# Kernel tuning notes

Hardware: AMD Instinct MI355X
Metric: run time of the kernel (lower is better)

## Reference

```python
import jax, jax.numpy as jnp
import numpy as np

S = 7
M = 8        # ensemble size (num_models)
D = 1008     # AEV feature dim
N = 50400    # total atoms (single conformer), divisible by S
LAYER_DIMS = (1008, 256, 192, 160, 1)
CELU_ALPHA = 0.1


def setup_inputs() -> dict:
    key = jax.random.key(0)
    ks = jax.random.split(key, 2 + 2 * (len(LAYER_DIMS) - 1))
    # Equal-size species groups (7200 atoms per species), randomly permuted.
    sp = jnp.tile(jnp.arange(S, dtype=jnp.int32), N // S)
    sp = jax.random.permutation(ks[0], sp)[None, :]                 # [1, N]
    aev = jax.random.normal(ks[1], (1, N, D), dtype=jnp.float32)    # [1, N, D]
    inp = {"species": sp, "aev": aev}
    for i in range(len(LAYER_DIMS) - 1):
        fan_in, fan_out = LAYER_DIMS[i], LAYER_DIMS[i + 1]
        w = jax.random.normal(ks[2 + 2 * i], (S, M, fan_in, fan_out), jnp.float32) / np.float32(np.sqrt(fan_in))
        b = jax.random.normal(ks[3 + 2 * i], (S, M, 1, fan_out), jnp.float32) * 0.01
        inp[f"W{i}"] = w
        inp[f"b{i}"] = b
    return inp


def _celu(x, alpha=CELU_ALPHA):
    return jnp.where(x > 0, x, alpha * jnp.expm1(x / alpha))


def _forward(species, aev, Ws, bs):
    sp = species.reshape(-1)                         # [N]
    x = aev.reshape(-1, aev.shape[-1])               # [N, D]
    s = Ws[0].shape[0]
    n = sp.shape[0]
    g = n // s                                       # atoms per species (equal groups)
    # MoE dispatch: stable sort by species -> contiguous equal-size blocks.
    order = jnp.argsort(sp)                          # [N]
    h = x[order].reshape(s, g, -1)                   # [S, G, D]
    # Fused per-species ensemble MLP (grouped batched GEMM = baddbmm per species).
    h = jnp.einsum('sgd,smdh->smgh', h, Ws[0]) + bs[0]   # [S, M, G, H0]
    for w, b in zip(Ws[1:], bs[1:]):
        h = _celu(h)
        h = jnp.einsum('smgh,smhp->smgp', h, w) + b
    atom_e = jnp.mean(h, axis=1)                     # mean over ensemble -> [S, G, 1]
    # Combine: scatter-sum of per-atom energies -> single molecular energy.
    return jnp.sum(atom_e).reshape(1)


def reference(species, aev, W0, b0, W1, b1, W2, b2, W3, b3):
    return _forward(species, aev, (W0, W1, W2, W3), (b0, b1, b2, b3))
```

## Files before the change

### kernel.cpp

```cpp
#include <hip/hip_runtime.h>
#include <cstdint>
#include <cstddef>

typedef unsigned short u16t;
typedef __attribute__((ext_vector_type(8))) short short8;
typedef __attribute__((ext_vector_type(4))) float float4v;

#define NATOMS 50400
#define SSP    7
#define DIN    1008
#define KP     1024
#define GRP    7200
#define GPAD   7296
#define H0D    256
#define H1D    192
#define H2D    160

#define OFF_CNT   0ull
#define OFF_SRC   256ull
#define OFF_X     204544ull
#define OFF_W0T   104800000ull
#define OFF_W1T   134160128ull
#define OFF_W2T   139665152ull

__device__ __forceinline__ u16t f2bf(float f) {
    union { float f; unsigned u; } x; x.f = f;
    unsigned r = x.u + 0x7fffu + ((x.u >> 16) & 1u);
    return (u16t)(r >> 16);
}
__device__ __forceinline__ float bf2f(u16t h) {
    return __uint_as_float(((unsigned)h) << 16);
}
__device__ __forceinline__ float celu_f(float x) {
    return x > 0.f ? x : 0.1f * (__expf(x * 10.f) - 1.f);
}
__device__ __forceinline__ void gll16(const void* g, void* l) {
    __builtin_amdgcn_global_load_lds(
        (const __attribute__((address_space(1))) void*)g,
        (__attribute__((address_space(3))) void*)l, 16, 0, 0);
}


__global__ void assign_k(const int* __restrict__ sp, int* __restrict__ cnt,
                         int* __restrict__ src_of) {
    int i = blockIdx.x * 256 + threadIdx.x;
    int lane = threadIdx.x & 63;
    int s = (i < NATOMS) ? sp[i] : -1;
#pragma unroll
    for (int t = 0; t < SSP; ++t) {
        unsigned long long m = __ballot(s == t);
        if (s == t) {
            int leader = __ffsll((unsigned long long)m) - 1;
            int rank = __popcll(m & ((1ull << lane) - 1ull));
            int base = 0;
            if (lane == leader) base = atomicAdd(&cnt[t], __popcll(m));
            base = __shfl(base, leader);
            src_of[t * GPAD + base + rank] = i;
        }
    }
}

__global__ void gather_k(const float* __restrict__ aev, const int* __restrict__ src_of,
                         u16t* __restrict__ X) {
    int wv = threadIdx.x >> 6, lane = threadIdx.x & 63;
    int s = blockIdx.y;
    int r = blockIdx.x * 4 + wv;
    int b = s * GPAD + r;
    bool valid = (r < GRP);
    int src = valid ? src_of[b] : 0;
    const float* ap = aev + (size_t)src * DIN;
    u16t* xp = X + (size_t)b * KP;
#pragma unroll
    for (int j = 0; j < 2; ++j) {
        int c = (j * 64 + lane) * 8;
        short8 o = (short8){0, 0, 0, 0, 0, 0, 0, 0};
        if (valid && c < DIN) {
            float4 v0 = *(const float4*)(ap + c);
            float4 v1 = *(const float4*)(ap + c + 4);
            o[0] = (short)f2bf(v0.x); o[1] = (short)f2bf(v0.y);
            o[2] = (short)f2bf(v0.z); o[3] = (short)f2bf(v0.w);
            o[4] = (short)f2bf(v1.x); o[5] = (short)f2bf(v1.y);
            o[6] = (short)f2bf(v1.z); o[7] = (short)f2bf(v1.w);
        }
        *(short8*)(xp + c) = o;
    }
}

__global__ void transpose_convert_k(const float* __restrict__ src, u16t* __restrict__ dst,
                                    int K_in, int C, int K_out) {
    __shared__ float tile[64][65];
    int b = blockIdx.z;
    int k0 = blockIdx.x * 64, c0 = blockIdx.y * 64;
    int tx = threadIdx.x & 63, ty = threadIdx.x >> 6;
    const float* sp = src + (size_t)b * K_in * C;
#pragma unroll
    for (int i = 0; i < 16; ++i) {
        int kl = i * 4 + ty;
        int k = k0 + kl, c = c0 + tx;
        float v = (k < K_in && c < C) ? sp[(size_t)k * C + c] : 0.f;
        tile[kl][tx] = v;
    }
    __syncthreads();
    u16t* dp = dst + (size_t)b * C * K_out;
    int kq = (threadIdx.x & 15) * 4;
    int cb = threadIdx.x >> 4;
#pragma unroll
    for (int p = 0; p < 4; ++p) {
        int cl = p * 16 + cb;
        int c = c0 + cl;
        if (c < C) {
            ushort4 o;
            o.x = f2bf(tile[kq + 0][cl]); o.y = f2bf(tile[kq + 1][cl]);
            o.z = f2bf(tile[kq + 2][cl]); o.w = f2bf(tile[kq + 3][cl]);
            *(ushort4*)(dp + (size_t)c * K_out + k0 + kq) = o;
        }
    }
}

__launch_bounds__(256, 2)
__global__ void fused(const u16t* __restrict__ X, const u16t* __restrict__ W0T,
                      const u16t* __restrict__ W1T, const u16t* __restrict__ W2T,
                      const float* __restrict__ b0, const float* __restrict__ b1,
                      const float* __restrict__ b2, const float* __restrict__ b3,
                      const float* __restrict__ W3, float* __restrict__ out) {
    __shared__ __attribute__((aligned(16))) char lbuf[65536];
    __shared__ float red[4];

    const int mtile = blockIdx.x + (blockIdx.y << 3);
    if (mtile >= GPAD / 128) return;
    const int bsm = blockIdx.z;

    const int tid = threadIdx.x, w = tid >> 6, lane = tid & 63;
    const int l15 = lane & 15, quad = lane >> 4;
    const int s = bsm >> 3;
    const int wr = w & 1, wc = w >> 1;

    const u16t* Xp = X + ((size_t)s * GPAD + (size_t)mtile * 128) * KP;
    const u16t* Wp = W0T + (size_t)bsm * H0D * KP;

    const u16t* gA[4]; const u16t* gB[8];
#pragma unroll
    for (int j = 0; j < 4; ++j) {
        int u = j * 256 + tid;
        int r = u >> 3, cs = (u & 7) ^ (r & 7);
        gA[j] = Xp + (size_t)r * KP + cs * 8;
    }
#pragma unroll
    for (int j = 0; j < 8; ++j) {
        int u = j * 256 + tid;
        int r = u >> 3, cs = (u & 7) ^ (r & 7);
        gB[j] = Wp + (size_t)r * KP + cs * 8;
    }
    int aoff[4][2], boff[8][2];
#pragma unroll
    for (int rt = 0; rt < 4; ++rt) {
        int r = wr * 64 + rt * 16 + l15;
#pragma unroll
        for (int ks = 0; ks < 2; ++ks)
            aoff[rt][ks] = r * 128 + (((ks * 4 + quad) ^ (r & 7)) * 16);
    }
#pragma unroll
    for (int ct = 0; ct < 8; ++ct) {
        int c = wc * 128 + ct * 16 + l15;
#pragma unroll
        for (int ks = 0; ks < 2; ++ks)
            boff[ct][ks] = c * 128 + (((ks * 4 + quad) ^ (c & 7)) * 16);
    }

    float4v acc[4][8];
#pragma unroll
    for (int i = 0; i < 4; ++i)
#pragma unroll
        for (int j = 0; j < 8; ++j) acc[i][j] = (float4v){0.f, 0.f, 0.f, 0.f};

    for (int kt = 0; kt < 16; ++kt) {
        const int ko = kt * 64;
        __syncthreads();
#pragma unroll
        for (int j = 0; j < 4; ++j) gll16(gA[j] + ko, lbuf + j * 4096 + w * 1024);
#pragma unroll
        for (int j = 0; j < 8; ++j) gll16(gB[j] + ko, lbuf + 16384 + j * 4096 + w * 1024);
        __syncthreads();
#pragma unroll
        for (int ks = 0; ks < 2; ++ks) {
            short8 a[4], b[8];
#pragma unroll
            for (int rt = 0; rt < 4; ++rt) a[rt] = *(const short8*)(lbuf + aoff[rt][ks]);
#pragma unroll
            for (int ct = 0; ct < 8; ++ct) b[ct] = *(const short8*)(lbuf + 16384 + boff[ct][ks]);
#pragma unroll
            for (int rt = 0; rt < 4; ++rt)
#pragma unroll
                for (int ct = 0; ct < 8; ++ct)
                    acc[rt][ct] = __builtin_amdgcn_mfma_f32_16x16x32_bf16(a[rt], b[ct], acc[rt][ct], 0, 0, 0);
        }
    }
    __syncthreads();

    {
        float bias[8];
#pragma unroll
        for (int ct = 0; ct < 8; ++ct)
            bias[ct] = b0[bsm * H0D + wc * 128 + ct * 16 + l15];
#pragma unroll
        for (int rt = 0; rt < 4; ++rt)
#pragma unroll
            for (int ct = 0; ct < 8; ++ct) {
                int col = wc * 128 + ct * 16 + l15;
                int ch = col >> 3;
#pragma unroll
                for (int rg = 0; rg < 4; ++rg) {
                    int row = wr * 64 + rt * 16 + quad * 4 + rg;
                    int sw = (ch & 24) | ((ch ^ row) & 7);
                    *(u16t*)(lbuf + row * 512 + sw * 16 + (col & 7) * 2) =
                        f2bf(celu_f(acc[rt][ct][rg] + bias[ct]));
                }
            }
    }

    const u16t* W1p = W1T + (size_t)bsm * H1D * H0D;
    const u16t* W2p = W2T + (size_t)bsm * H2D * H1D;
    const u16t* bp1[6];
#pragma unroll
    for (int ct = 0; ct < 6; ++ct)
        bp1[ct] = W1p + (size_t)(wc * 96 + ct * 16 + l15) * H0D + quad * 8;
    short8 bc[6];
#pragma unroll
    for (int ct = 0; ct < 6; ++ct) bc[ct] = *(const short8*)(bp1[ct]);

    __syncthreads();

    float4v acc2[4][6];
#pragma unroll
    for (int i = 0; i < 4; ++i)
#pragma unroll
        for (int j = 0; j < 6; ++j) acc2[i][j] = (float4v){0.f, 0.f, 0.f, 0.f};

    for (int kc = 0; kc < 8; ++kc) {
        const int kn = ((kc + 1 < 8) ? kc + 1 : kc) * 32;
        short8 a[4];
#pragma unroll
        for (int rt = 0; rt < 4; ++rt) {
            int r = wr * 64 + rt * 16 + l15;
            int ch = kc * 4 + quad;
            int sw = (ch & 24) | ((ch ^ r) & 7);
            a[rt] = *(const short8*)(lbuf + r * 512 + sw * 16);
        }
        short8 bn[6];
#pragma unroll
        for (int ct = 0; ct < 6; ++ct) bn[ct] = *(const short8*)(bp1[ct] + kn);
#pragma unroll
        for (int rt = 0; rt < 4; ++rt)
#pragma unroll
            for (int ct = 0; ct < 6; ++ct)
                acc2[rt][ct] = __builtin_amdgcn_mfma_f32_16x16x32_bf16(a[rt], bc[ct], acc2[rt][ct], 0, 0, 0);
#pragma unroll
        for (int ct = 0; ct < 6; ++ct) bc[ct] = bn[ct];
    }

    const u16t* bp2[5];
#pragma unroll
    for (int ct = 0; ct < 5; ++ct)
        bp2[ct] = W2p + (size_t)(wc * 80 + ct * 16 + l15) * H1D + quad * 8;
    short8 bc3[5];
#pragma unroll
    for (int ct = 0; ct < 5; ++ct) bc3[ct] = *(const short8*)(bp2[ct]);

    __syncthreads();

    {
        float bias[6];
#pragma unroll
        for (int ct = 0; ct < 6; ++ct) bias[ct] = b1[bsm * H1D + wc * 96 + ct * 16 + l15];
#pragma unroll
        for (int rt = 0; rt < 4; ++rt)
#pragma unroll
            for (int ct = 0; ct < 6; ++ct) {
                int h = wc * 96 + ct * 16 + l15;
                int ch = h >> 3;
#pragma unroll
                for (int rg = 0; rg < 4; ++rg) {
                    int g = wr * 64 + rt * 16 + quad * 4 + rg;
                    float v = celu_f(acc2[rt][ct][rg] + bias[ct]);
                    int sw = (ch & ~7) | ((ch ^ g) & 7);
                    *(u16t*)(lbuf + g * 384 + sw * 16 + (h & 7) * 2) = f2bf(v);
                }
            }
    }
    __syncthreads();

    float4v acc3[4][5];
#pragma unroll
    for (int i = 0; i < 4; ++i)
#pragma unroll
        for (int j = 0; j < 5; ++j) acc3[i][j] = (float4v){0.f, 0.f, 0.f, 0.f};

    for (int kc = 0; kc < 6; ++kc) {
        const int kn = ((kc + 1 < 6) ? kc + 1 : kc) * 32;
        short8 a[4];
#pragma unroll
        for (int rt = 0; rt < 4; ++rt) {
            int r = wr * 64 + rt * 16 + l15;
            int ch = kc * 4 + quad;
            int sw = (ch & ~7) | ((ch ^ r) & 7);
            a[rt] = *(const short8*)(lbuf + r * 384 + sw * 16);
        }
        short8 bn[5];
#pragma unroll
        for (int ct = 0; ct < 5; ++ct) bn[ct] = *(const short8*)(bp2[ct] + kn);
#pragma unroll
        for (int rt = 0; rt < 4; ++rt)
#pragma unroll
            for (int ct = 0; ct < 5; ++ct)
                acc3[rt][ct] = __builtin_amdgcn_mfma_f32_16x16x32_bf16(a[rt], bc3[ct], acc3[rt][ct], 0, 0, 0);
#pragma unroll
        for (int ct = 0; ct < 5; ++ct) bc3[ct] = bn[ct];
    }

    {
        float b2r[5], w3r[5];
#pragma unroll
        for (int ct = 0; ct < 5; ++ct) {
            int col = wc * 80 + ct * 16 + l15;
            b2r[ct] = b2[bsm * H2D + col];
            w3r[ct] = W3[bsm * H2D + col];
        }
        float sum = 0.f;
#pragma unroll
        for (int rt = 0; rt < 4; ++rt)
#pragma unroll
            for (int rg = 0; rg < 4; ++rg) {
                int row = mtile * 128 + wr * 64 + rt * 16 + quad * 4 + rg;
                if (row < GRP) {
#pragma unroll
                    for (int ct = 0; ct < 5; ++ct)
                        sum += celu_f(acc3[rt][ct][rg] + b2r[ct]) * w3r[ct];
                }
            }
#pragma unroll
        for (int off = 32; off; off >>= 1) sum += __shfl_xor(sum, off);
        if (lane == 0) red[w] = sum;
    }
    __syncthreads();
    if (tid == 0) {
        int nv = GRP - mtile * 128; nv = nv < 0 ? 0 : (nv > 128 ? 128 : nv);
        atomicAdd(out, (red[0] + red[1] + red[2] + red[3] + (float)nv * b3[bsm]) * 0.125f);
    }
}

extern "C" void kernel_launch(void* const* d_in, const int* in_sizes, int n_in,
                              void* d_out, int out_size, void* d_ws, size_t ws_size,
                              hipStream_t stream) {
    const int*   species = (const int*)d_in[0];
    const float* aev     = (const float*)d_in[1];
    const float* W0      = (const float*)d_in[2];
    const float* b0      = (const float*)d_in[3];
    const float* W1      = (const float*)d_in[4];
    const float* b1      = (const float*)d_in[5];
    const float* W2      = (const float*)d_in[6];
    const float* b2      = (const float*)d_in[7];
    const float* W3      = (const float*)d_in[8];
    const float* b3      = (const float*)d_in[9];
    float* out = (float*)d_out;
    char*  ws  = (char*)d_ws;

    int*  cnt    = (int*)(ws + OFF_CNT);
    int*  src_of = (int*)(ws + OFF_SRC);
    u16t* X      = (u16t*)(ws + OFF_X);
    u16t* W0T    = (u16t*)(ws + OFF_W0T);
    u16t* W1T    = (u16t*)(ws + OFF_W1T);
    u16t* W2T    = (u16t*)(ws + OFF_W2T);

    hipMemsetAsync(cnt, 0, 32, stream);
    hipMemsetAsync(d_out, 0, sizeof(float), stream);

    assign_k<<<(NATOMS + 255) / 256, 256, 0, stream>>>(species, cnt, src_of);
    gather_k<<<dim3(GPAD / 4, SSP), 256, 0, stream>>>(aev, src_of, X);
    transpose_convert_k<<<dim3(16, 4, 56), 256, 0, stream>>>(W0, W0T, DIN, H0D, KP);
    transpose_convert_k<<<dim3(4, 3, 56), 256, 0, stream>>>(W1, W1T, H0D, H1D, H0D);
    transpose_convert_k<<<dim3(3, 3, 56), 256, 0, stream>>>(W2, W2T, H1D, H2D, H1D);

    fused<<<dim3(8, 8, 56), 256, 0, stream>>>(X, W0T, W1T, W2T,
                                              b0, b1, b2, b3, W3, out);
}
```

Baseline: 805.9 us.

## Double-buffer W0 tiles in LDS and load X operands directly to registers

The layer-0 GEMM loop now keeps the weight tile in two LDS buffers, prefetching two k-steps ahead with direct global-to-LDS loads and explicit waitcnt/barrier control in place of two __syncthreads per step. The activation (X) operand is no longer staged through LDS; each wave loads its MFMA A fragments straight from global memory into registers, one k-step ahead. This is meant to overlap global latency with MFMA work and cut LDS traffic and synchronisation. The cost is more register pressure, which may lower occupancy, and uncoalesced row-strided global reads for X.

Measured after the change: 924.5 us. 14.7% more time.

```diff
diff --git a/kernel.cpp b/kernel.cpp
--- a/kernel.cpp
+++ b/kernel.cpp
@@ -138,27 +138,11 @@
     const u16t* Xp = X + ((size_t)s * GPAD + (size_t)mtile * 128) * KP;
     const u16t* Wp = W0T + (size_t)bsm * H0D * KP;
 
-    const u16t* gA[4]; const u16t* gB[8];
-#pragma unroll
-    for (int j = 0; j < 4; ++j) {
-        int u = j * 256 + tid;
-        int r = u >> 3, cs = (u & 7) ^ (r & 7);
-        gA[j] = Xp + (size_t)r * KP + cs * 8;
-    }
-#pragma unroll
-    for (int j = 0; j < 8; ++j) {
-        int u = j * 256 + tid;
-        int r = u >> 3, cs = (u & 7) ^ (r & 7);
-        gB[j] = Wp + (size_t)r * KP + cs * 8;
-    }
-    int aoff[4][2], boff[8][2];
-#pragma unroll
-    for (int rt = 0; rt < 4; ++rt) {
-        int r = wr * 64 + rt * 16 + l15;
-#pragma unroll
-        for (int ks = 0; ks < 2; ++ks)
-            aoff[rt][ks] = r * 128 + (((ks * 4 + quad) ^ (r & 7)) * 16);
-    }
+    const u16t* abase = Xp + (size_t)(wr * 64 + l15) * KP + quad * 8;
+    const int r0 = tid >> 3, c0s = (tid & 7) ^ (r0 & 7);
+    const u16t* gB0 = Wp + (size_t)r0 * KP + c0s * 8;
+
+    int boff[8][2];
 #pragma unroll
     for (int ct = 0; ct < 8; ++ct) {
         int c = wc * 128 + ct * 16 + l15;
@@ -173,29 +157,56 @@
 #pragma unroll
         for (int j = 0; j < 8; ++j) acc[i][j] = (float4v){0.f, 0.f, 0.f, 0.f};
 
+    short8 a[4][2];
+#pragma unroll
+    for (int rt = 0; rt < 4; ++rt)
+#pragma unroll
+        for (int ks = 0; ks < 2; ++ks)
+            a[rt][ks] = *(const short8*)(abase + (size_t)rt * 16 * KP + ks * 32);
+#pragma unroll
+    for (int j = 0; j < 8; ++j)
+        gll16(gB0 + (size_t)j * 32 * KP, lbuf + j * 4096 + w * 1024);
+#pragma unroll
+    for (int j = 0; j < 8; ++j)
+        gll16(gB0 + (size_t)j * 32 * KP + 64, lbuf + 32768 + j * 4096 + w * 1024);
+    asm volatile("s_waitcnt vmcnt(8)" ::: "memory");
+    __builtin_amdgcn_s_barrier();
+
+    int cur = 0;
     for (int kt = 0; kt < 16; ++kt) {
-        const int ko = kt * 64;
-        __syncthreads();
-#pragma unroll
-        for (int j = 0; j < 4; ++j) gll16(gA[j] + ko, lbuf + j * 4096 + w * 1024);
-#pragma unroll
-        for (int j = 0; j < 8; ++j) gll16(gB[j] + ko, lbuf + 16384 + j * 4096 + w * 1024);
-        __syncthreads();
+        const char* bb = lbuf + cur * 32768;
 #pragma unroll
         for (int ks = 0; ks < 2; ++ks) {
-            short8 a[4], b[8];
-#pragma unroll
-            for (int rt = 0; rt < 4; ++rt) a[rt] = *(const short8*)(lbuf + aoff[rt][ks]);
-#pragma unroll
-            for (int ct = 0; ct < 8; ++ct) b[ct] = *(const short8*)(lbuf + 16384 + boff[ct][ks]);
+            short8 b[8];
+#pragma unroll
+            for (int ct = 0; ct < 8; ++ct) b[ct] = *(const short8*)(bb + boff[ct][ks]);
 #pragma unroll
             for (int rt = 0; rt < 4; ++rt)
 #pragma unroll
                 for (int ct = 0; ct < 8; ++ct)
-                    acc[rt][ct] = __builtin_amdgcn_mfma_f32_16x16x32_bf16(a[rt], b[ct], acc[rt][ct], 0, 0, 0);
-        }
-    }
-    __syncthreads();
+                    acc[rt][ct] = __builtin_amdgcn_mfma_f32_16x16x32_bf16(a[rt][ks], b[ct], acc[rt][ct], 0, 0, 0);
+        }
+        {
+            const int kn = (kt < 15 ? kt + 1 : 15) * 64;
+#pragma unroll
+            for (int rt = 0; rt < 4; ++rt)
+#pragma unroll
+                for (int ks = 0; ks < 2; ++ks)
+                    a[rt][ks] = *(const short8*)(abase + (size_t)rt * 16 * KP + kn + ks * 32);
+        }
+        asm volatile("s_waitcnt lgkmcnt(0)" ::: "memory");
+        __builtin_amdgcn_s_barrier();
+        if (kt < 14) {
+            const int ko = (kt + 2) * 64;
+#pragma unroll
+            for (int j = 0; j < 8; ++j)
+                gll16(gB0 + (size_t)j * 32 * KP + ko,
+                      lbuf + cur * 32768 + j * 4096 + w * 1024);
+        }
+        asm volatile("s_waitcnt vmcnt(8)" ::: "memory");
+        __builtin_amdgcn_s_barrier();
+        cur ^= 1;
+    }
 
     {
         float bias[8];
@@ -238,13 +249,13 @@
 
     for (int kc = 0; kc < 8; ++kc) {
         const int kn = ((kc + 1 < 8) ? kc + 1 : kc) * 32;
-        short8 a[4];
+        short8 a2[4];
 #pragma unroll
         for (int rt = 0; rt < 4; ++rt) {
             int r = wr * 64 + rt * 16 + l15;
             int ch = kc * 4 + quad;
             int sw = (ch & 24) | ((ch ^ r) & 7);
-            a[rt] = *(const short8*)(lbuf + r * 512 + sw * 16);
+            a2[rt] = *(const short8*)(lbuf + r * 512 + sw * 16);
         }
         short8 bn[6];
 #pragma unroll
@@ -253,7 +264,7 @@
         for (int rt = 0; rt < 4; ++rt)
 #pragma unroll
             for (int ct = 0; ct < 6; ++ct)
-                acc2[rt][ct] = __builtin_amdgcn_mfma_f32_16x16x32_bf16(a[rt], bc[ct], acc2[rt][ct], 0, 0, 0);
+                acc2[rt][ct] = __builtin_amdgcn_mfma_f32_16x16x32_bf16(a2[rt], bc[ct], acc2[rt][ct], 0, 0, 0);
 #pragma unroll
         for (int ct = 0; ct < 6; ++ct) bc[ct] = bn[ct];
     }
@@ -297,13 +308,13 @@
 
     for (int kc = 0; kc < 6; ++kc) {
         const int kn = ((kc + 1 < 6) ? kc + 1 : kc) * 32;
-        short8 a[4];
+        short8 a3[4];
 #pragma unroll
         for (int rt = 0; rt < 4; ++rt) {
             int r = wr * 64 + rt * 16 + l15;
             int ch = kc * 4 + quad;
             int sw = (ch & ~7) | ((ch ^ r) & 7);
-            a[rt] = *(const short8*)(lbuf + r * 384 + sw * 16);
+            a3[rt] = *(const short8*)(lbuf + r * 384 + sw * 16);
         }
         short8 bn[5];
 #pragma unroll
@@ -312,7 +323,7 @@
         for (int rt = 0; rt < 4; ++rt)
 #pragma unroll
             for (int ct = 0; ct < 5; ++ct)
-                acc3[rt][ct] = __builtin_amdgcn_mfma_f32_16x16x32_bf16(a[rt], bc3[ct], acc3[rt][ct], 0, 0, 0);
+                acc3[rt][ct] = __builtin_amdgcn_mfma_f32_16x16x32_bf16(a3[rt], bc3[ct], acc3[rt][ct], 0, 0, 0);
 #pragma unroll
         for (int ct = 0; ct < 5; ++ct) bc3[ct] = bn[ct];
     }
```

## Use 512-thread blocks with eight waves splitting the fused MLP tiles

Applied to the files above, without the earlier changes.

The fused MLP kernel now runs 512 threads (8 waves) per block instead of 256, with launch bounds (512,4). Each wave holds half as many accumulators in all three GEMM stages: layer 0 uses a 2x4 wave grid with 4x4 MFMA tiles, and layers 1-2 use a 4x2 grid with two row tiles per wave. The global-to-LDS loads are redistributed to match. The intent is to cut per-wave register pressure and add waves to hide latency, at the cost of more barrier participants and less register-level reuse per wave.

Result: slower. 983.6 us (+22.0%).

```diff
diff --git a/kernel.cpp b/kernel.cpp
--- a/kernel.cpp
+++ b/kernel.cpp
@@ -117,14 +117,14 @@
     }
 }
 
-__launch_bounds__(256, 2)
+__launch_bounds__(512, 4)
 __global__ void fused(const u16t* __restrict__ X, const u16t* __restrict__ W0T,
                       const u16t* __restrict__ W1T, const u16t* __restrict__ W2T,
                       const float* __restrict__ b0, const float* __restrict__ b1,
                       const float* __restrict__ b2, const float* __restrict__ b3,
                       const float* __restrict__ W3, float* __restrict__ out) {
     __shared__ __attribute__((aligned(16))) char lbuf[65536];
-    __shared__ float red[4];
+    __shared__ float red[8];
 
     const int mtile = blockIdx.x + (blockIdx.y << 3);
     if (mtile >= GPAD / 128) return;
@@ -134,79 +134,69 @@
     const int l15 = lane & 15, quad = lane >> 4;
     const int s = bsm >> 3;
     const int wr = w & 1, wc = w >> 1;
+    const int wr2 = w & 3, wc2 = w >> 2;
 
     const u16t* Xp = X + ((size_t)s * GPAD + (size_t)mtile * 128) * KP;
     const u16t* Wp = W0T + (size_t)bsm * H0D * KP;
 
-    const u16t* gA[4]; const u16t* gB[8];
-#pragma unroll
-    for (int j = 0; j < 4; ++j) {
-        int u = j * 256 + tid;
-        int r = u >> 3, cs = (u & 7) ^ (r & 7);
-        gA[j] = Xp + (size_t)r * KP + cs * 8;
-    }
-#pragma unroll
-    for (int j = 0; j < 8; ++j) {
-        int u = j * 256 + tid;
-        int r = u >> 3, cs = (u & 7) ^ (r & 7);
-        gB[j] = Wp + (size_t)r * KP + cs * 8;
-    }
-    int aoff[4][2], boff[8][2];
+    const int r0 = tid >> 3, c0s = (tid & 7) ^ (r0 & 7);
+    const u16t* gA0 = Xp + (size_t)r0 * KP + c0s * 8;
+    const u16t* gB0 = Wp + (size_t)r0 * KP + c0s * 8;
+
+    int aoff[4], boff[4];
 #pragma unroll
     for (int rt = 0; rt < 4; ++rt) {
         int r = wr * 64 + rt * 16 + l15;
-#pragma unroll
-        for (int ks = 0; ks < 2; ++ks)
-            aoff[rt][ks] = r * 128 + (((ks * 4 + quad) ^ (r & 7)) * 16);
-    }
-#pragma unroll
-    for (int ct = 0; ct < 8; ++ct) {
-        int c = wc * 128 + ct * 16 + l15;
-#pragma unroll
-        for (int ks = 0; ks < 2; ++ks)
-            boff[ct][ks] = c * 128 + (((ks * 4 + quad) ^ (c & 7)) * 16);
-    }
-
-    float4v acc[4][8];
+        aoff[rt] = r * 128 + ((quad ^ (r & 7)) * 16);
+    }
+#pragma unroll
+    for (int ct = 0; ct < 4; ++ct) {
+        int c = wc * 64 + ct * 16 + l15;
+        boff[ct] = c * 128 + ((quad ^ (c & 7)) * 16);
+    }
+
+    float4v acc[4][4];
 #pragma unroll
     for (int i = 0; i < 4; ++i)
 #pragma unroll
-        for (int j = 0; j < 8; ++j) acc[i][j] = (float4v){0.f, 0.f, 0.f, 0.f};
+        for (int j = 0; j < 4; ++j) acc[i][j] = (float4v){0.f, 0.f, 0.f, 0.f};
 
     for (int kt = 0; kt < 16; ++kt) {
         const int ko = kt * 64;
         __syncthreads();
-#pragma unroll
-        for (int j = 0; j < 4; ++j) gll16(gA[j] + ko, lbuf + j * 4096 + w * 1024);
-#pragma unroll
-        for (int j = 0; j < 8; ++j) gll16(gB[j] + ko, lbuf + 16384 + j * 4096 + w * 1024);
+        gll16(gA0 + ko, lbuf + w * 1024);
+        gll16(gA0 + (size_t)64 * KP + ko, lbuf + 8192 + w * 1024);
+#pragma unroll
+        for (int j = 0; j < 4; ++j)
+            gll16(gB0 + (size_t)j * 64 * KP + ko, lbuf + 16384 + j * 8192 + w * 1024);
         __syncthreads();
 #pragma unroll
         for (int ks = 0; ks < 2; ++ks) {
-            short8 a[4], b[8];
-#pragma unroll
-            for (int rt = 0; rt < 4; ++rt) a[rt] = *(const short8*)(lbuf + aoff[rt][ks]);
-#pragma unroll
-            for (int ct = 0; ct < 8; ++ct) b[ct] = *(const short8*)(lbuf + 16384 + boff[ct][ks]);
+            const int kx = ks * 64;
+            short8 a[4], b[4];
+#pragma unroll
+            for (int rt = 0; rt < 4; ++rt) a[rt] = *(const short8*)(lbuf + (aoff[rt] ^ kx));
+#pragma unroll
+            for (int ct = 0; ct < 4; ++ct) b[ct] = *(const short8*)(lbuf + 16384 + (boff[ct] ^ kx));
 #pragma unroll
             for (int rt = 0; rt < 4; ++rt)
 #pragma unroll
-                for (int ct = 0; ct < 8; ++ct)
+                for (int ct = 0; ct < 4; ++ct)
                     acc[rt][ct] = __builtin_amdgcn_mfma_f32_16x16x32_bf16(a[rt], b[ct], acc[rt][ct], 0, 0, 0);
         }
     }
     __syncthreads();
 
     {
-        float bias[8];
-#pragma unroll
-        for (int ct = 0; ct < 8; ++ct)
-            bias[ct] = b0[bsm * H0D + wc * 128 + ct * 16 + l15];
+        float bias[4];
+#pragma unroll
+        for (int ct = 0; ct < 4; ++ct)
+            bias[ct] = b0[bsm * H0D + wc * 64 + ct * 16 + l15];
 #pragma unroll
         for (int rt = 0; rt < 4; ++rt)
 #pragma unroll
-            for (int ct = 0; ct < 8; ++ct) {
-                int col = wc * 128 + ct * 16 + l15;
+            for (int ct = 0; ct < 4; ++ct) {
+                int col = wc * 64 + ct * 16 + l15;
                 int ch = col >> 3;
 #pragma unroll
                 for (int rg = 0; rg < 4; ++rg) {
@@ -223,37 +213,37 @@
     const u16t* bp1[6];
 #pragma unroll
     for (int ct = 0; ct < 6; ++ct)
-        bp1[ct] = W1p + (size_t)(wc * 96 + ct * 16 + l15) * H0D + quad * 8;
+        bp1[ct] = W1p + (size_t)(wc2 * 96 + ct * 16 + l15) * H0D + quad * 8;
     short8 bc[6];
 #pragma unroll
     for (int ct = 0; ct < 6; ++ct) bc[ct] = *(const short8*)(bp1[ct]);
 
     __syncthreads();
 
-    float4v acc2[4][6];
-#pragma unroll
-    for (int i = 0; i < 4; ++i)
+    float4v acc2[2][6];
+#pragma unroll
+    for (int i = 0; i < 2; ++i)
 #pragma unroll
         for (int j = 0; j < 6; ++j) acc2[i][j] = (float4v){0.f, 0.f, 0.f, 0.f};
 
     for (int kc = 0; kc < 8; ++kc) {
         const int kn = ((kc + 1 < 8) ? kc + 1 : kc) * 32;
-        short8 a[4];
-#pragma unroll
-        for (int rt = 0; rt < 4; ++rt) {
-            int r = wr * 64 + rt * 16 + l15;
+        short8 a2[2];
+#pragma unroll
+        for (int rt = 0; rt < 2; ++rt) {
+            int r = wr2 * 32 + rt * 16 + l15;
             int ch = kc * 4 + quad;
             int sw = (ch & 24) | ((ch ^ r) & 7);
-            a[rt] = *(const short8*)(lbuf + r * 512 + sw * 16);
+            a2[rt] = *(const short8*)(lbuf + r * 512 + sw * 16);
         }
         short8 bn[6];
 #pragma unroll
         for (int ct = 0; ct < 6; ++ct) bn[ct] = *(const short8*)(bp1[ct] + kn);
 #pragma unroll
-        for (int rt = 0; rt < 4; ++rt)
+        for (int rt = 0; rt < 2; ++rt)
 #pragma unroll
             for (int ct = 0; ct < 6; ++ct)
-                acc2[rt][ct] = __builtin_amdgcn_mfma_f32_16x16x32_bf16(a[rt], bc[ct], acc2[rt][ct], 0, 0, 0);
+                acc2[rt][ct] = __builtin_amdgcn_mfma_f32_16x16x32_bf16(a2[rt], bc[ct], acc2[rt][ct], 0, 0, 0);
 #pragma unroll
         for (int ct = 0; ct < 6; ++ct) bc[ct] = bn[ct];
     }
@@ -261,7 +251,7 @@
     const u16t* bp2[5];
 #pragma unroll
     for (int ct = 0; ct < 5; ++ct)
-        bp2[ct] = W2p + (size_t)(wc * 80 + ct * 16 + l15) * H1D + quad * 8;
+        bp2[ct] = W2p + (size_t)(wc2 * 80 + ct * 16 + l15) * H1D + quad * 8;
     short8 bc3[5];
 #pragma unroll
     for (int ct = 0; ct < 5; ++ct) bc3[ct] = *(const short8*)(bp2[ct]);
@@ -271,16 +261,16 @@
     {
         float bias[6];
 #pragma unroll
-        for (int ct = 0; ct < 6; ++ct) bias[ct] = b1[bsm * H1D + wc * 96 + ct * 16 + l15];
-#pragma unroll
-        for (int rt = 0; rt < 4; ++rt)
+        for (int ct = 0; ct < 6; ++ct) bias[ct] = b1[bsm * H1D + wc2 * 96 + ct * 16 + l15];
+#pragma unroll
+        for (int rt = 0; rt < 2; ++rt)
 #pragma unroll
             for (int ct = 0; ct < 6; ++ct) {
-                int h = wc * 96 + ct * 16 + l15;
+                int h = wc2 * 96 + ct * 16 + l15;
                 int ch = h >> 3;
 #pragma unroll
                 for (int rg = 0; rg < 4; ++rg) {
-                    int g = wr * 64 + rt * 16 + quad * 4 + rg;
+                    int g = wr2 * 32 + rt * 16 + quad * 4 + rg;
                     float v = celu_f(acc2[rt][ct][rg] + bias[ct]);
                     int sw = (ch & ~7) | ((ch ^ g) & 7);
                     *(u16t*)(lbuf + g * 384 + sw * 16 + (h & 7) * 2) = f2bf(v);
@@ -289,30 +279,30 @@
     }
     __syncthreads();
 
-    float4v acc3[4][5];
-#pragma unroll
-    for (int i = 0; i < 4; ++i)
+    float4v acc3[2][5];
+#pragma unroll
+    for (int i = 0; i < 2; ++i)
 #pragma unroll
         for (int j = 0; j < 5; ++j) acc3[i][j] = (float4v){0.f, 0.f, 0.f, 0.f};
 
     for (int kc = 0; kc < 6; ++kc) {
         const int kn = ((kc + 1 < 6) ? kc + 1 : kc) * 32;
-        short8 a[4];
-#pragma unroll
-        for (int rt = 0; rt < 4; ++rt) {
-            int r = wr * 64 + rt * 16 + l15;
+        short8 a3[2];
+#pragma unroll
+        for (int rt = 0; rt < 2; ++rt) {
+            int r = wr2 * 32 + rt * 16 + l15;
             int ch = kc * 4 + quad;
             int sw = (ch & ~7) | ((ch ^ r) & 7);
-            a[rt] = *(const short8*)(lbuf + r * 384 + sw * 16);
+            a3[rt] = *(const short8*)(lbuf + r * 384 + sw * 16);
         }
         short8 bn[5];
 #pragma unroll
         for (int ct = 0; ct < 5; ++ct) bn[ct] = *(const short8*)(bp2[ct] + kn);
 #pragma unroll
-        for (int rt = 0; rt < 4; ++rt)
+        for (int rt = 0; rt < 2; ++rt)
 #pragma unroll
             for (int ct = 0; ct < 5; ++ct)
-                acc3[rt][ct] = __builtin_amdgcn_mfma_f32_16x16x32_bf16(a[rt], bc3[ct], acc3[rt][ct], 0, 0, 0);
+                acc3[rt][ct] = __builtin_amdgcn_mfma_f32_16x16x32_bf16(a3[rt], bc3[ct], acc3[rt][ct], 0, 0, 0);
 #pragma unroll
         for (int ct = 0; ct < 5; ++ct) bc3[ct] = bn[ct];
     }
@@ -321,16 +311,16 @@
         float b2r[5], w3r[5];
 #pragma unroll
         for (int ct = 0; ct < 5; ++ct) {
-            int col = wc * 80 + ct * 16 + l15;
+            int col = wc2 * 80 + ct * 16 + l15;
             b2r[ct] = b2[bsm * H2D + col];
             w3r[ct] = W3[bsm * H2D + col];
         }
         float sum = 0.f;
 #pragma unroll
-        for (int rt = 0; rt < 4; ++rt)
+        for (int rt = 0; rt < 2; ++rt)
 #pragma unroll
             for (int rg = 0; rg < 4; ++rg) {
-                int row = mtile * 128 + wr * 64 + rt * 16 + quad * 4 + rg;
+                int row = mtile * 128 + wr2 * 32 + rt * 16 + quad * 4 + rg;
                 if (row < GRP) {
 #pragma unroll
                     for (int ct = 0; ct < 5; ++ct)
@@ -344,7 +334,9 @@
     __syncthreads();
     if (tid == 0) {
         int nv = GRP - mtile * 128; nv = nv < 0 ? 0 : (nv > 128 ? 128 : nv);
-        atomicAdd(out, (red[0] + red[1] + red[2] + red[3] + (float)nv * b3[bsm]) * 0.125f);
+        float t = red[0] + red[1] + red[2] + red[3] +
+                  red[4] + red[5] + red[6] + red[7];
+        atomicAdd(out, (t + (float)nv * b3[bsm]) * 0.125f);
     }
 }
 
@@ -380,6 +372,6 @@
     transpose_convert_k<<<dim3(4, 3, 56), 256, 0, stream>>>(W1, W1T, H0D, H1D, H0D);
     transpose_convert_k<<<dim3(3, 3, 56), 256, 0, stream>>>(W2, W2T, H1D, H2D, H1D);
 
-    fused<<<dim3(8, 8, 56), 256, 0, stream>>>(X, W0T, W1T, W2T,
+    fused<<<dim3(8, 8, 56), 512, 0, stream>>>(X, W0T, W1T, W2T,
                                               b0, b1, b2, b3, W3, out);
 }
```
